# Performance work log

Hardware: AMD Instinct MI355X
Metric: run time of the kernel (lower is better)

The kernel has to match this reference:

```python
import jax, jax.numpy as jnp
import numpy as np

N = 50000   # nodes
E = 800000  # edges (avg degree 16)
D = 128     # in_feats == out_feats


def setup_inputs() -> dict:
    key = jax.random.key(0)
    k1, k2, k3, k4 = jax.random.split(key, 4)
    h = jax.random.normal(k1, (N, D), dtype=jnp.float32)
    src = jax.random.randint(k2, (E,), 0, N, dtype=jnp.int32)
    dst = jax.random.randint(k3, (E,), 0, N, dtype=jnp.int32)
    snorm_n = jnp.ones((N, 1), dtype=jnp.float32)  # sqrt(1/N) replicated; identity-scaled here
    # NodeApply linear: Linear(2*D, D) with bias
    W = jax.random.normal(k4, (D, 2 * D), dtype=jnp.float32) / np.sqrt(2 * D).astype(np.float32)
    b = jnp.zeros((D,), dtype=jnp.float32)
    return {"h": h, "snorm_n": snorm_n, "W": W, "b": b, "src": src, "dst": dst}


def reference(h, snorm_n, W, b, src, dst):
    # dropout p=0.0 -> identity
    h_in = h
    # gather neighbor messages and segment-mean aggregate (MeanAggregator)
    ones = jnp.ones((src.shape[0],), dtype=h.dtype)
    deg = jax.ops.segment_sum(ones, dst, num_segments=N)            # [N]
    msg_sum = jax.ops.segment_sum(h[src], dst, num_segments=N)     # [N, D]
    c = msg_sum / jnp.maximum(deg, 1.0)[:, None]                   # zero-degree nodes -> c = 0
    # NodeApply: concat -> linear -> L2 normalize -> relu
    bundle = jnp.concatenate([h, c], axis=1) @ W.T + b             # [N, D]
    nrm = jnp.sqrt(jnp.sum(bundle * bundle, axis=1, keepdims=True))
    bundle = bundle / jnp.maximum(nrm, 1e-12)                      # F.normalize(p=2, dim=1)
    out = jax.nn.relu(bundle)
    # graph norm
    out = out * snorm_n
    # residual (in_feats == out_feats)
    return h_in + out
```

## Files before the change

kernel.cpp:

```cpp
#include <hip/hip_runtime.h>
#include <hip/hip_bf16.h>

#define TPB 256
#define CHUNK_LOG 13
#define CHUNK (1 << CHUNK_LOG)
#define HSTRIDE 12544

typedef __attribute__((ext_vector_type(8))) short bf16x8;
typedef __attribute__((ext_vector_type(4))) float f32x4;
typedef __attribute__((ext_vector_type(2))) float f32x2;

__device__ inline unsigned short f2bf(float f) {
    unsigned u = __float_as_uint(f);
    unsigned r = u + 0x7fffu + ((u >> 16) & 1u);
    return (unsigned short)(r >> 16);
}
__device__ inline float bf2f(unsigned short s) {
    return __uint_as_float(((unsigned)s) << 16);
}

__global__ void k_hist(const int* __restrict__ dst,
                       unsigned* __restrict__ hist32, unsigned char* __restrict__ lrank,
                       int E) {
    __shared__ unsigned lhist[HSTRIDE];
    int b = blockIdx.x;
    for (int i = threadIdx.x; i < HSTRIDE; i += TPB) lhist[i] = 0;
    __syncthreads();
    int e0 = b << CHUNK_LOG;
    int e1 = min(e0 + CHUNK, E);
    for (int e = e0 + (int)threadIdx.x; e < e1; e += TPB) {
        int d = dst[e];
        unsigned sh = (d & 3) * 8;
        unsigned old = atomicAdd(&lhist[d >> 2], 1u << sh);
        lrank[e] = (unsigned char)((old >> sh) & 0xffu);
    }
    __syncthreads();
    for (int i = threadIdx.x; i < HSTRIDE; i += TPB)
        hist32[(size_t)b * HSTRIDE + i] = lhist[i];
}

__launch_bounds__(TPB)
__global__ void k_scan(const unsigned* __restrict__ hist32,
                       unsigned short* __restrict__ cbase,
                       int* __restrict__ bsum, unsigned* ctr,
                       int* __restrict__ offs, int N, int E, int NBH) {
    extern __shared__ unsigned tile[];
    __shared__ int sdata[4];
    __shared__ int sb[TPB];
    __shared__ int wsum[4];
    int NB = gridDim.x;
    int bid = blockIdx.x, tid = threadIdx.x;
    int lane = tid & 63, w = tid >> 6;

    int tileBase = bid * 64;
    int total = NBH * 64;
    for (int i = tid; i < total; i += TPB) {
        int b = i >> 6, c = i & 63;
        tile[i] = hist32[(size_t)b * HSTRIDE + tileBase + c];
    }
    __syncthreads();
    int n = bid * TPB + tid;
    unsigned sh = (tid & 3) * 8;
    int wcol = tid >> 2;
    int run = 0;
    for (int b = 0; b < NBH; ++b) {
        int c = (int)((tile[b * 64 + wcol] >> sh) & 0xffu);
        if (n < N) cbase[(size_t)b * N + n] = (unsigned short)run;
        run += c;
    }
    int dv = (n < N) ? run : 0;

    int s = dv;
    for (int o = 32; o; o >>= 1) s += __shfl_xor(s, o);
    if (lane == 0) sdata[w] = s;
    __syncthreads();
    if (tid == 0) {
        int tot = sdata[0] + sdata[1] + sdata[2] + sdata[3];
        __hip_atomic_store(&bsum[bid], tot, __ATOMIC_RELAXED, __HIP_MEMORY_SCOPE_AGENT);
        __hip_atomic_fetch_add(ctr, 1u, __ATOMIC_RELEASE, __HIP_MEMORY_SCOPE_AGENT);
        while (__hip_atomic_load(ctr, __ATOMIC_ACQUIRE, __HIP_MEMORY_SCOPE_AGENT)
               < (unsigned)NB)
            __builtin_amdgcn_s_sleep(2);
    }
    __syncthreads();

    int v = 0;
    if (tid < NB)
        v = __hip_atomic_load(&bsum[tid], __ATOMIC_RELAXED, __HIP_MEMORY_SCOPE_AGENT);
    int x = v;
    for (int o = 1; o < 64; o <<= 1) { int y = __shfl_up(x, o); if (lane >= o) x += y; }
    if (lane == 63) wsum[w] = x;
    __syncthreads();
    int add = 0;
    for (int k = 0; k < w; ++k) add += wsum[k];
    sb[tid] = add + x - v;
    __syncthreads();
    int base = sb[bid];

    int y2 = dv;
    for (int o = 1; o < 64; o <<= 1) { int z = __shfl_up(y2, o); if (lane >= o) y2 += z; }
    __syncthreads();
    if (lane == 63) wsum[w] = y2;
    __syncthreads();
    int add2 = 0;
    for (int k = 0; k < w; ++k) add2 += wsum[k];
    int ex = base + add2 + y2 - dv;
    if (n < N) offs[n] = ex;
    if (n == N - 1) offs[N] = E;
}

__global__ void k_scatterconv(const float* __restrict__ h, const float* __restrict__ W,
                              const int* __restrict__ src, const int* __restrict__ dst,
                              const unsigned char* __restrict__ lrank,
                              const unsigned short* __restrict__ cbase,
                              const int* __restrict__ offs,
                              unsigned short* __restrict__ esrc,
                              unsigned short* __restrict__ h_hi,
                              unsigned* __restrict__ h8,
                              unsigned short* __restrict__ Wb,
                              int N, int E, int nchunk) {
    int nh4 = N * 32;
    int totalc = nh4 + 8192;
    for (int t = blockIdx.x * TPB + threadIdx.x; t < totalc; t += gridDim.x * TPB) {
        if (t < nh4) {
            float4 v = ((const float4*)h)[t];
            ushort4 hi;
            hi.x = f2bf(v.x); hi.y = f2bf(v.y);
            hi.z = f2bf(v.z); hi.w = f2bf(v.w);
            ((ushort4*)h_hi)[t] = hi;
            int p8 = __builtin_amdgcn_cvt_pk_fp8_f32(v.x, v.y, 0, false);
            p8 = __builtin_amdgcn_cvt_pk_fp8_f32(v.z, v.w, p8, true);
            h8[t] = (unsigned)p8;
        } else {
            int w4 = t - nh4;
            float4 v = ((const float4*)W)[w4];
            ushort4 hi;
            hi.x = f2bf(v.x); hi.y = f2bf(v.y);
            hi.z = f2bf(v.z); hi.w = f2bf(v.w);
            ((ushort4*)Wb)[w4] = hi;
        }
    }
    int slice = blockIdx.x & 7;
    int chunk = blockIdx.x >> 3;
    int lo = (int)((long long)N * slice >> 3);
    int hi = (int)((long long)N * (slice + 1) >> 3);
    for (int e = chunk * TPB + threadIdx.x; e < E; e += nchunk * TPB) {
        int d = dst[e];
        if (d >= lo && d < hi) {
            int b = e >> CHUNK_LOG;
            int pos = offs[d] + (int)cbase[(size_t)b * N + d] + (int)lrank[e];
            esrc[pos] = (unsigned short)src[e];
        }
    }
}

__global__ void k_agg(const unsigned* __restrict__ h8, const int* __restrict__ offs,
                      const unsigned short* __restrict__ esrc,
                      unsigned* __restrict__ c, int N) {
    int wav = (blockIdx.x * TPB + threadIdx.x) >> 6;
    int half = (threadIdx.x >> 5) & 1;
    int hl = threadIdx.x & 31;
    int n = wav * 2 + half;
    if (n >= N) return;
    int beg = offs[n], end = offs[n + 1];
    float a0 = 0.f, a1 = 0.f, a2 = 0.f, a3 = 0.f;
    int e = beg;
    for (; e + 3 < end; e += 4) {
        int s0 = esrc[e], s1 = esrc[e + 1], s2 = esrc[e + 2], s3 = esrc[e + 3];
        unsigned u0 = h8[(size_t)s0 * 32 + hl];
        unsigned u1 = h8[(size_t)s1 * 32 + hl];
        unsigned u2 = h8[(size_t)s2 * 32 + hl];
        unsigned u3 = h8[(size_t)s3 * 32 + hl];
        f32x2 p0 = __builtin_amdgcn_cvt_pk_f32_fp8((int)u0, false);
        f32x2 q0 = __builtin_amdgcn_cvt_pk_f32_fp8((int)u0, true);
        f32x2 p1 = __builtin_amdgcn_cvt_pk_f32_fp8((int)u1, false);
        f32x2 q1 = __builtin_amdgcn_cvt_pk_f32_fp8((int)u1, true);
        f32x2 p2 = __builtin_amdgcn_cvt_pk_f32_fp8((int)u2, false);
        f32x2 q2 = __builtin_amdgcn_cvt_pk_f32_fp8((int)u2, true);
        f32x2 p3 = __builtin_amdgcn_cvt_pk_f32_fp8((int)u3, false);
        f32x2 q3 = __builtin_amdgcn_cvt_pk_f32_fp8((int)u3, true);
        a0 += p0.x + p1.x + p2.x + p3.x;
        a1 += p0.y + p1.y + p2.y + p3.y;
        a2 += q0.x + q1.x + q2.x + q3.x;
        a3 += q0.y + q1.y + q2.y + q3.y;
    }
    for (; e < end; ++e) {
        unsigned u0 = h8[(size_t)esrc[e] * 32 + hl];
        f32x2 p0 = __builtin_amdgcn_cvt_pk_f32_fp8((int)u0, false);
        f32x2 q0 = __builtin_amdgcn_cvt_pk_f32_fp8((int)u0, true);
        a0 += p0.x; a1 += p0.y; a2 += q0.x; a3 += q0.y;
    }
    float inv = 1.0f / fmaxf((float)(end - beg), 1.0f);
    unsigned pk0 = ((unsigned)f2bf(a1 * inv) << 16) | (unsigned)f2bf(a0 * inv);
    unsigned pk1 = ((unsigned)f2bf(a3 * inv) << 16) | (unsigned)f2bf(a2 * inv);
    c[(size_t)n * 64 + hl * 2]     = pk0;
    c[(size_t)n * 64 + hl * 2 + 1] = pk1;
}

__launch_bounds__(TPB)
__global__ void k_apply(const unsigned short* __restrict__ h_hi,
                        const unsigned short* __restrict__ c,
                        const unsigned short* __restrict__ Wb,
                        const float* __restrict__ bia,
                        const float* __restrict__ snorm,
                        float* __restrict__ out, int N) {
    int lane = threadIdx.x & 63;
    int l15 = lane & 15, l4 = lane >> 4;
    int wave = threadIdx.x >> 6;
    int r0 = blockIdx.x * 128 + wave * 32;

    f32x4 acc[2][8] = {};

    #pragma unroll
    for (int kc = 0; kc < 8; ++kc) {
        bf16x8 Bf[8];
        #pragma unroll
        for (int n = 0; n < 8; ++n) {
            Bf[n] = *(const bf16x8*)((const char*)Wb +
                     ((size_t)(n * 16 + l15) * 512 + (size_t)kc * 64 + (size_t)l4 * 16));
        }
        #pragma unroll
        for (int rf = 0; rf < 2; ++rf) {
            int row = r0 + rf * 16 + l15;
            if (row > N - 1) row = N - 1;
            bf16x8 av;
            if (kc < 4) {
                av = *(const bf16x8*)((const char*)h_hi +
                      ((size_t)row * 256 + (size_t)kc * 64 + (size_t)l4 * 16));
            } else {
                av = *(const bf16x8*)((const char*)c +
                      ((size_t)row * 256 + (size_t)(kc - 4) * 64 + (size_t)l4 * 16));
            }
            #pragma unroll
            for (int n = 0; n < 8; ++n)
                acc[rf][n] = __builtin_amdgcn_mfma_f32_16x16x32_bf16(av, Bf[n], acc[rf][n], 0, 0, 0);
        }
    }

    float bn[8];
    #pragma unroll
    for (int n = 0; n < 8; ++n) bn[n] = bia[n * 16 + l15];

    #pragma unroll
    for (int rf = 0; rf < 2; ++rf) {
        float sq[4] = {0.f, 0.f, 0.f, 0.f};
        #pragma unroll
        for (int n = 0; n < 8; ++n) {
            #pragma unroll
            for (int g = 0; g < 4; ++g) {
                acc[rf][n][g] += bn[n];
                sq[g] += acc[rf][n][g] * acc[rf][n][g];
            }
        }
        #pragma unroll
        for (int g = 0; g < 4; ++g) {
            sq[g] += __shfl_xor(sq[g], 1);
            sq[g] += __shfl_xor(sq[g], 2);
            sq[g] += __shfl_xor(sq[g], 4);
            sq[g] += __shfl_xor(sq[g], 8);
        }
        #pragma unroll
        for (int g = 0; g < 4; ++g) {
            int row = r0 + rf * 16 + l4 * 4 + g;
            if (row < N) {
                float invn = 1.0f / fmaxf(sqrtf(sq[g]), 1e-12f);
                float sn = snorm[row];
                #pragma unroll
                for (int n = 0; n < 8; ++n) {
                    int col = n * 16 + l15;
                    float res = bf2f(h_hi[(size_t)row * 128 + col]);
                    out[(size_t)row * 128 + col] =
                        fmaxf(acc[rf][n][g] * invn, 0.f) * sn + res;
                }
            }
        }
    }
}

extern "C" void kernel_launch(void* const* d_in, const int* in_sizes, int n_in,
                              void* d_out, int out_size, void* d_ws, size_t ws_size,
                              hipStream_t stream) {
    const float* h     = (const float*)d_in[0];
    const float* snorm = (const float*)d_in[1];
    const float* W     = (const float*)d_in[2];
    const float* b     = (const float*)d_in[3];
    const int*   src   = (const int*)d_in[4];
    const int*   dst   = (const int*)d_in[5];
    int N = in_sizes[1];
    int E = in_sizes[4];
    float* out = (float*)d_out;

    char* ws = (char*)d_ws;
    size_t off = 0;
    auto alloc = [&](size_t bytes) {
        void* ptr = ws + off;
        off = (off + bytes + 255) & ~(size_t)255;
        return ptr;
    };
    int NB  = (N + TPB - 1) / TPB;
    int NBH = (E + CHUNK - 1) >> CHUNK_LOG;
    int* offs   = (int*)alloc((size_t)(N + 1) * 4);
    int* bsum   = (int*)alloc((size_t)NB * 4);
    unsigned* ctr          = (unsigned*)alloc(256);
    unsigned* hist32       = (unsigned*)alloc((size_t)NBH * HSTRIDE * 4);
    unsigned short* cbase  = (unsigned short*)alloc((size_t)NBH * N * 2);
    unsigned char*  lrank  = (unsigned char*)alloc((size_t)E);
    unsigned short* esrc   = (unsigned short*)alloc((size_t)E * 2);
    unsigned short* h_hi   = (unsigned short*)alloc((size_t)N * 128 * 2);
    unsigned*       h8     = (unsigned*)alloc((size_t)N * 128);
    unsigned short* Wb     = (unsigned short*)alloc((size_t)128 * 256 * 2);
    unsigned* c = hist32;

    hipMemsetAsync(ctr, 0, 4, stream);

    k_hist<<<NBH, TPB, 0, stream>>>(dst, hist32, lrank, E);

    size_t tile_bytes = (size_t)NBH * 64 * 4;
    k_scan<<<NB, TPB, tile_bytes, stream>>>(hist32, cbase, bsum, ctr, offs, N, E, NBH);

    int nchunk = 512;
    k_scatterconv<<<8 * nchunk, TPB, 0, stream>>>(h, W, src, dst, lrank, cbase, offs,
                                                  esrc, h_hi, h8, Wb, N, E, nchunk);

    int aggblk = (N + 7) / 8;
    k_agg<<<aggblk, TPB, 0, stream>>>(h8, offs, esrc, c, N);

    int nblk = (N + 127) / 128;
    k_apply<<<nblk, TPB, 0, stream>>>(h_hi, (const unsigned short*)c, Wb, b, snorm, out, N);
}
```

Baseline: 109.9 us.

## Fold counter reset into hist kernel, unroll aggregation by 8, nontemporal output stores

Drops the separate hipMemsetAsync by having block 0 of k_hist zero the scan counter, saving one stream operation. The gather loop in k_agg is unrolled from 4 to 8 edges to keep more independent loads in flight, and the sums use a pairwise tree. Final output stores in k_apply become nontemporal to avoid polluting the cache. The unroll raises register pressure and routes more edges through the scalar tail loop for average degree 16.

Result: faster. 106.7 us (-2.9%).

```diff
diff --git a/kernel.cpp b/kernel.cpp
--- a/kernel.cpp
+++ b/kernel.cpp
@@ -21,9 +21,10 @@
 
 __global__ void k_hist(const int* __restrict__ dst,
                        unsigned* __restrict__ hist32, unsigned char* __restrict__ lrank,
-                       int E) {
+                       unsigned* ctr, int E) {
     __shared__ unsigned lhist[HSTRIDE];
     int b = blockIdx.x;
+    if (b == 0 && threadIdx.x == 0) *ctr = 0u;
     for (int i = threadIdx.x; i < HSTRIDE; i += TPB) lhist[i] = 0;
     __syncthreads();
     int e0 = b << CHUNK_LOG;
@@ -165,12 +166,15 @@
     int beg = offs[n], end = offs[n + 1];
     float a0 = 0.f, a1 = 0.f, a2 = 0.f, a3 = 0.f;
     int e = beg;
-    for (; e + 3 < end; e += 4) {
-        int s0 = esrc[e], s1 = esrc[e + 1], s2 = esrc[e + 2], s3 = esrc[e + 3];
-        unsigned u0 = h8[(size_t)s0 * 32 + hl];
-        unsigned u1 = h8[(size_t)s1 * 32 + hl];
-        unsigned u2 = h8[(size_t)s2 * 32 + hl];
-        unsigned u3 = h8[(size_t)s3 * 32 + hl];
+    for (; e + 7 < end; e += 8) {
+        unsigned u0 = h8[(size_t)esrc[e]     * 32 + hl];
+        unsigned u1 = h8[(size_t)esrc[e + 1] * 32 + hl];
+        unsigned u2 = h8[(size_t)esrc[e + 2] * 32 + hl];
+        unsigned u3 = h8[(size_t)esrc[e + 3] * 32 + hl];
+        unsigned u4 = h8[(size_t)esrc[e + 4] * 32 + hl];
+        unsigned u5 = h8[(size_t)esrc[e + 5] * 32 + hl];
+        unsigned u6 = h8[(size_t)esrc[e + 6] * 32 + hl];
+        unsigned u7 = h8[(size_t)esrc[e + 7] * 32 + hl];
         f32x2 p0 = __builtin_amdgcn_cvt_pk_f32_fp8((int)u0, false);
         f32x2 q0 = __builtin_amdgcn_cvt_pk_f32_fp8((int)u0, true);
         f32x2 p1 = __builtin_amdgcn_cvt_pk_f32_fp8((int)u1, false);
@@ -179,10 +183,18 @@
         f32x2 q2 = __builtin_amdgcn_cvt_pk_f32_fp8((int)u2, true);
         f32x2 p3 = __builtin_amdgcn_cvt_pk_f32_fp8((int)u3, false);
         f32x2 q3 = __builtin_amdgcn_cvt_pk_f32_fp8((int)u3, true);
-        a0 += p0.x + p1.x + p2.x + p3.x;
-        a1 += p0.y + p1.y + p2.y + p3.y;
-        a2 += q0.x + q1.x + q2.x + q3.x;
-        a3 += q0.y + q1.y + q2.y + q3.y;
+        f32x2 p4 = __builtin_amdgcn_cvt_pk_f32_fp8((int)u4, false);
+        f32x2 q4 = __builtin_amdgcn_cvt_pk_f32_fp8((int)u4, true);
+        f32x2 p5 = __builtin_amdgcn_cvt_pk_f32_fp8((int)u5, false);
+        f32x2 q5 = __builtin_amdgcn_cvt_pk_f32_fp8((int)u5, true);
+        f32x2 p6 = __builtin_amdgcn_cvt_pk_f32_fp8((int)u6, false);
+        f32x2 q6 = __builtin_amdgcn_cvt_pk_f32_fp8((int)u6, true);
+        f32x2 p7 = __builtin_amdgcn_cvt_pk_f32_fp8((int)u7, false);
+        f32x2 q7 = __builtin_amdgcn_cvt_pk_f32_fp8((int)u7, true);
+        a0 += (p0.x + p1.x) + (p2.x + p3.x) + (p4.x + p5.x) + (p6.x + p7.x);
+        a1 += (p0.y + p1.y) + (p2.y + p3.y) + (p4.y + p5.y) + (p6.y + p7.y);
+        a2 += (q0.x + q1.x) + (q2.x + q3.x) + (q4.x + q5.x) + (q6.x + q7.x);
+        a3 += (q0.y + q1.y) + (q2.y + q3.y) + (q4.y + q5.y) + (q6.y + q7.y);
     }
     for (; e < end; ++e) {
         unsigned u0 = h8[(size_t)esrc[e] * 32 + hl];
@@ -269,8 +281,8 @@
                 for (int n = 0; n < 8; ++n) {
                     int col = n * 16 + l15;
                     float res = bf2f(h_hi[(size_t)row * 128 + col]);
-                    out[(size_t)row * 128 + col] =
-                        fmaxf(acc[rf][n][g] * invn, 0.f) * sn + res;
+                    float v = fmaxf(acc[rf][n][g] * invn, 0.f) * sn + res;
+                    __builtin_nontemporal_store(v, &out[(size_t)row * 128 + col]);
                 }
             }
         }
@@ -311,9 +323,7 @@
     unsigned short* Wb     = (unsigned short*)alloc((size_t)128 * 256 * 2);
     unsigned* c = hist32;
 
-    hipMemsetAsync(ctr, 0, 4, stream);
-
-    k_hist<<<NBH, TPB, 0, stream>>>(dst, hist32, lrank, E);
+    k_hist<<<NBH, TPB, 0, stream>>>(dst, hist32, lrank, ctr, E);
 
     size_t tile_bytes = (size_t)NBH * 64 * 4;
     k_scan<<<NB, TPB, tile_bytes, stream>>>(hist32, cbase, bsum, ctr, offs, N, E, NBH);
```

## Store aggregated features as fp8, software-pipeline gather, drop memset, nontemporal output

Applied to the files above, without the earlier changes.

The aggregation kernel now prefetches the next 8 neighbor indices while gathering the current 8 rows, so index loads overlap the feature gathers. The mean-aggregated vector is written as fp8 instead of bf16, halving that intermediate's traffic, and the apply kernel expands it back to bf16 before the MFMA. The counter memset is folded into the histogram kernel, removing one stream operation, and output stores use nontemporal hints. Storing the mean in fp8 loses precision in the linear layer's second half.

After: 102.4 us (median of 2 runs). 6.8% less time.

```diff
diff --git a/kernel.cpp b/kernel.cpp
--- a/kernel.cpp
+++ b/kernel.cpp
@@ -21,9 +21,10 @@
 
 __global__ void k_hist(const int* __restrict__ dst,
                        unsigned* __restrict__ hist32, unsigned char* __restrict__ lrank,
-                       int E) {
+                       unsigned* ctr, int E) {
     __shared__ unsigned lhist[HSTRIDE];
     int b = blockIdx.x;
+    if (b == 0 && threadIdx.x == 0) *ctr = 0u;
     for (int i = threadIdx.x; i < HSTRIDE; i += TPB) lhist[i] = 0;
     __syncthreads();
     int e0 = b << CHUNK_LOG;
@@ -154,52 +155,73 @@
     }
 }
 
+#define AGG_ACC(u)                                                            \
+    {                                                                         \
+        f32x2 _p = __builtin_amdgcn_cvt_pk_f32_fp8((int)(u), false);          \
+        f32x2 _q = __builtin_amdgcn_cvt_pk_f32_fp8((int)(u), true);           \
+        a0 += _p.x; a1 += _p.y; a2 += _q.x; a3 += _q.y;                       \
+    }
+
 __global__ void k_agg(const unsigned* __restrict__ h8, const int* __restrict__ offs,
                       const unsigned short* __restrict__ esrc,
-                      unsigned* __restrict__ c, int N) {
+                      unsigned* __restrict__ c8, int N) {
     int wav = (blockIdx.x * TPB + threadIdx.x) >> 6;
     int half = (threadIdx.x >> 5) & 1;
     int hl = threadIdx.x & 31;
     int n = wav * 2 + half;
     if (n >= N) return;
     int beg = offs[n], end = offs[n + 1];
+    int cnt = end - beg;
     float a0 = 0.f, a1 = 0.f, a2 = 0.f, a3 = 0.f;
     int e = beg;
-    for (; e + 3 < end; e += 4) {
-        int s0 = esrc[e], s1 = esrc[e + 1], s2 = esrc[e + 2], s3 = esrc[e + 3];
+    int s0 = 0, s1 = 0, s2 = 0, s3 = 0, s4 = 0, s5 = 0, s6 = 0, s7 = 0;
+    if (cnt >= 8) {
+        s0 = esrc[e];     s1 = esrc[e + 1]; s2 = esrc[e + 2]; s3 = esrc[e + 3];
+        s4 = esrc[e + 4]; s5 = esrc[e + 5]; s6 = esrc[e + 6]; s7 = esrc[e + 7];
+    }
+    while (cnt >= 16) {
+        int t0 = esrc[e + 8],  t1 = esrc[e + 9],  t2 = esrc[e + 10], t3 = esrc[e + 11];
+        int t4 = esrc[e + 12], t5 = esrc[e + 13], t6 = esrc[e + 14], t7 = esrc[e + 15];
         unsigned u0 = h8[(size_t)s0 * 32 + hl];
         unsigned u1 = h8[(size_t)s1 * 32 + hl];
         unsigned u2 = h8[(size_t)s2 * 32 + hl];
         unsigned u3 = h8[(size_t)s3 * 32 + hl];
-        f32x2 p0 = __builtin_amdgcn_cvt_pk_f32_fp8((int)u0, false);
-        f32x2 q0 = __builtin_amdgcn_cvt_pk_f32_fp8((int)u0, true);
-        f32x2 p1 = __builtin_amdgcn_cvt_pk_f32_fp8((int)u1, false);
-        f32x2 q1 = __builtin_amdgcn_cvt_pk_f32_fp8((int)u1, true);
-        f32x2 p2 = __builtin_amdgcn_cvt_pk_f32_fp8((int)u2, false);
-        f32x2 q2 = __builtin_amdgcn_cvt_pk_f32_fp8((int)u2, true);
-        f32x2 p3 = __builtin_amdgcn_cvt_pk_f32_fp8((int)u3, false);
-        f32x2 q3 = __builtin_amdgcn_cvt_pk_f32_fp8((int)u3, true);
-        a0 += p0.x + p1.x + p2.x + p3.x;
-        a1 += p0.y + p1.y + p2.y + p3.y;
-        a2 += q0.x + q1.x + q2.x + q3.x;
-        a3 += q0.y + q1.y + q2.y + q3.y;
-    }
-    for (; e < end; ++e) {
+        unsigned u4 = h8[(size_t)s4 * 32 + hl];
+        unsigned u5 = h8[(size_t)s5 * 32 + hl];
+        unsigned u6 = h8[(size_t)s6 * 32 + hl];
+        unsigned u7 = h8[(size_t)s7 * 32 + hl];
+        AGG_ACC(u0) AGG_ACC(u1) AGG_ACC(u2) AGG_ACC(u3)
+        AGG_ACC(u4) AGG_ACC(u5) AGG_ACC(u6) AGG_ACC(u7)
+        s0 = t0; s1 = t1; s2 = t2; s3 = t3;
+        s4 = t4; s5 = t5; s6 = t6; s7 = t7;
+        e += 8; cnt -= 8;
+    }
+    if (cnt >= 8) {
+        unsigned u0 = h8[(size_t)s0 * 32 + hl];
+        unsigned u1 = h8[(size_t)s1 * 32 + hl];
+        unsigned u2 = h8[(size_t)s2 * 32 + hl];
+        unsigned u3 = h8[(size_t)s3 * 32 + hl];
+        unsigned u4 = h8[(size_t)s4 * 32 + hl];
+        unsigned u5 = h8[(size_t)s5 * 32 + hl];
+        unsigned u6 = h8[(size_t)s6 * 32 + hl];
+        unsigned u7 = h8[(size_t)s7 * 32 + hl];
+        AGG_ACC(u0) AGG_ACC(u1) AGG_ACC(u2) AGG_ACC(u3)
+        AGG_ACC(u4) AGG_ACC(u5) AGG_ACC(u6) AGG_ACC(u7)
+        e += 8; cnt -= 8;
+    }
+    for (; cnt > 0; --cnt, ++e) {
         unsigned u0 = h8[(size_t)esrc[e] * 32 + hl];
-        f32x2 p0 = __builtin_amdgcn_cvt_pk_f32_fp8((int)u0, false);
-        f32x2 q0 = __builtin_amdgcn_cvt_pk_f32_fp8((int)u0, true);
-        a0 += p0.x; a1 += p0.y; a2 += q0.x; a3 += q0.y;
+        AGG_ACC(u0)
     }
     float inv = 1.0f / fmaxf((float)(end - beg), 1.0f);
-    unsigned pk0 = ((unsigned)f2bf(a1 * inv) << 16) | (unsigned)f2bf(a0 * inv);
-    unsigned pk1 = ((unsigned)f2bf(a3 * inv) << 16) | (unsigned)f2bf(a2 * inv);
-    c[(size_t)n * 64 + hl * 2]     = pk0;
-    c[(size_t)n * 64 + hl * 2 + 1] = pk1;
+    int pk = __builtin_amdgcn_cvt_pk_fp8_f32(a0 * inv, a1 * inv, 0, false);
+    pk = __builtin_amdgcn_cvt_pk_fp8_f32(a2 * inv, a3 * inv, pk, true);
+    c8[(size_t)n * 32 + hl] = (unsigned)pk;
 }
 
 __launch_bounds__(TPB)
 __global__ void k_apply(const unsigned short* __restrict__ h_hi,
-                        const unsigned short* __restrict__ c,
+                        const unsigned char* __restrict__ c8,
                         const unsigned short* __restrict__ Wb,
                         const float* __restrict__ bia,
                         const float* __restrict__ snorm,
@@ -228,8 +250,18 @@
                 av = *(const bf16x8*)((const char*)h_hi +
                       ((size_t)row * 256 + (size_t)kc * 64 + (size_t)l4 * 16));
             } else {
-                av = *(const bf16x8*)((const char*)c +
-                      ((size_t)row * 256 + (size_t)(kc - 4) * 64 + (size_t)l4 * 16));
+                uint2 cu = *(const uint2*)(c8 + (size_t)row * 128 +
+                            (size_t)(kc - 4) * 32 + (size_t)l4 * 8);
+                f32x2 p = __builtin_amdgcn_cvt_pk_f32_fp8((int)cu.x, false);
+                f32x2 q = __builtin_amdgcn_cvt_pk_f32_fp8((int)cu.x, true);
+                f32x2 r = __builtin_amdgcn_cvt_pk_f32_fp8((int)cu.y, false);
+                f32x2 s = __builtin_amdgcn_cvt_pk_f32_fp8((int)cu.y, true);
+                union { unsigned u[4]; bf16x8 v; } cv;
+                asm("v_cvt_pk_bf16_f32 %0, %1, %2" : "=v"(cv.u[0]) : "v"(p.x), "v"(p.y));
+                asm("v_cvt_pk_bf16_f32 %0, %1, %2" : "=v"(cv.u[1]) : "v"(q.x), "v"(q.y));
+                asm("v_cvt_pk_bf16_f32 %0, %1, %2" : "=v"(cv.u[2]) : "v"(r.x), "v"(r.y));
+                asm("v_cvt_pk_bf16_f32 %0, %1, %2" : "=v"(cv.u[3]) : "v"(s.x), "v"(s.y));
+                av = cv.v;
             }
             #pragma unroll
             for (int n = 0; n < 8; ++n)
@@ -269,8 +301,8 @@
                 for (int n = 0; n < 8; ++n) {
                     int col = n * 16 + l15;
                     float res = bf2f(h_hi[(size_t)row * 128 + col]);
-                    out[(size_t)row * 128 + col] =
-                        fmaxf(acc[rf][n][g] * invn, 0.f) * sn + res;
+                    float v = fmaxf(acc[rf][n][g] * invn, 0.f) * sn + res;
+                    __builtin_nontemporal_store(v, &out[(size_t)row * 128 + col]);
                 }
             }
         }
@@ -309,11 +341,9 @@
     unsigned short* h_hi   = (unsigned short*)alloc((size_t)N * 128 * 2);
     unsigned*       h8     = (unsigned*)alloc((size_t)N * 128);
     unsigned short* Wb     = (unsigned short*)alloc((size_t)128 * 256 * 2);
-    unsigned* c = hist32;
-
-    hipMemsetAsync(ctr, 0, 4, stream);
-
-    k_hist<<<NBH, TPB, 0, stream>>>(dst, hist32, lrank, E);
+    unsigned* c8 = hist32;
+
+    k_hist<<<NBH, TPB, 0, stream>>>(dst, hist32, lrank, ctr, E);
 
     size_t tile_bytes = (size_t)NBH * 64 * 4;
     k_scan<<<NB, TPB, tile_bytes, stream>>>(hist32, cbase, bsum, ctr, offs, N, E, NBH);
@@ -323,8 +353,8 @@
                                                   esrc, h_hi, h8, Wb, N, E, nchunk);
 
     int aggblk = (N + 7) / 8;
-    k_agg<<<aggblk, TPB, 0, stream>>>(h8, offs, esrc, c, N);
+    k_agg<<<aggblk, TPB, 0, stream>>>(h8, offs, esrc, c8, N);
 
     int nblk = (N + 127) / 128;
-    k_apply<<<nblk, TPB, 0, stream>>>(h_hi, (const unsigned short*)c, Wb, b, snorm, out, N);
-}
+    k_apply<<<nblk, TPB, 0, stream>>>(h_hi, (const unsigned char*)c8, Wb, b, snorm, out, N);
+}
```
